# Kernel tuning notes

Hardware: AMD Instinct MI355X
Metric: run time of the kernel (lower is better)

## Reference

```python
import jax, jax.numpy as jnp
import numpy as np

EPS = 1e-5  # nn.LayerNorm default eps
N_LAYERS, N, D_IN, H, D_OUT, NH = 4, 2048, 512, 1024, 256, 16


def setup_inputs() -> dict:
    key = jax.random.key(0)
    ks = jax.random.split(key, 8)
    s = lambda k, shape: (jax.random.normal(k, shape, jnp.float32) * 0.02)
    return {
        "x": jax.random.normal(ks[0], (N, D_IN), jnp.float32),
        "W1": s(ks[1], (H, D_IN)), "b1": jnp.zeros((H,), jnp.float32),
        # per-layer MHA params, stacked on a leading layer axis
        "Wqkv": s(ks[2], (N_LAYERS, 3 * H, H)), "bqkv": jnp.zeros((N_LAYERS, 3 * H), jnp.float32),
        "Wo": s(ks[3], (N_LAYERS, H, H)), "bo": jnp.zeros((N_LAYERS, H), jnp.float32),
        "ln_g": jnp.ones((N_LAYERS, H), jnp.float32), "ln_b": jnp.zeros((N_LAYERS, H), jnp.float32),
        "W2": s(ks[4], (D_OUT, H)), "b2": jnp.zeros((D_OUT,), jnp.float32),
        "g_out": jnp.ones((D_OUT,), jnp.float32), "b_out": jnp.zeros((D_OUT,), jnp.float32),
        "num_heads": NH,
    }


def layer_norm(x, g, b):
    m = jnp.mean(x, axis=-1, keepdims=True)
    v = jnp.mean(jnp.square(x - m), axis=-1, keepdims=True)
    return (x - m) * jax.lax.rsqrt(v + EPS) * g + b


def mha(x, Wqkv, bqkv, Wo, bo, nh):
    # x: [N, H]; attention is over the N axis (torch MHA with batch_first=False, batch=1)
    n, h = x.shape
    hd = h // nh
    qkv = x @ Wqkv.T + bqkv                      # [N, 3H]
    q, k, v = jnp.split(qkv, 3, axis=-1)
    q = q.reshape(n, nh, hd).transpose(1, 0, 2)  # [nh, N, hd]
    k = k.reshape(n, nh, hd).transpose(1, 0, 2)
    v = v.reshape(n, nh, hd).transpose(1, 0, 2)
    scale = jnp.float32(1.0 / np.sqrt(hd))
    scores = jnp.einsum('hnd,hmd->hnm', q, k) * scale  # [nh, N, N]
    attn = jax.nn.softmax(scores, axis=-1)
    out = jnp.einsum('hnm,hmd->hnd', attn, v)          # [nh, N, hd]
    out = out.transpose(1, 0, 2).reshape(n, h)
    return out @ Wo.T + bo


def reference(x, W1, b1, Wqkv, bqkv, Wo, bo, ln_g, ln_b, W2, b2, g_out, b_out, num_heads):
    h = jax.nn.relu(x @ W1.T + b1)  # dropout is identity in eval mode
    for i in range(Wqkv.shape[0]):
        a = mha(h, Wqkv[i], bqkv[i], Wo[i], bo[i], num_heads)
        h = layer_norm(a + h, ln_g[i], ln_b[i])
    y = jax.nn.relu(h @ W2.T + b2)
    return layer_norm(y, g_out, b_out)
```

## Files before the change

### kernel.cpp

```cpp
#include <hip/hip_runtime.h>

typedef __attribute__((ext_vector_type(8))) short short8;
typedef __attribute__((ext_vector_type(4))) float f32x4;
typedef __attribute__((ext_vector_type(16))) float f32x16;
typedef __attribute__((ext_vector_type(4))) float float4v;
typedef __attribute__((ext_vector_type(4))) unsigned short ushort4v;
typedef __attribute__((ext_vector_type(4))) unsigned int uint4v;
typedef __attribute__((ext_vector_type(2))) unsigned int uint2v;

#define MFMA16(a, b, c) __builtin_amdgcn_mfma_f32_16x16x32_bf16((a), (b), (c), 0, 0, 0)
#define MFMA32(a, b, c) __builtin_amdgcn_mfma_f32_32x32x16_bf16((a), (b), (c), 0, 0, 0)
#define GLOAD_LDS16(g, s)                                                         \
  __builtin_amdgcn_global_load_lds((const __attribute__((address_space(1))) void*)(g), \
                                   (__attribute__((address_space(3))) void*)(s), 16, 0, 0)
#define EXP2(x) __builtin_amdgcn_exp2f(x)

__device__ __forceinline__ unsigned short f2bf(float f) {
  unsigned u = __builtin_bit_cast(unsigned, f);
  u += 0x7fffu + ((u >> 16) & 1u);
  return (unsigned short)(u >> 16);
}

__device__ __forceinline__ unsigned cvtpk(float lo, float hi) {
  unsigned r;
  asm("v_cvt_pk_bf16_f32 %0, %1, %2" : "=v"(r) : "v"(lo), "v"(hi));
  return r;
}

__device__ __forceinline__ void swap32(unsigned& a, unsigned& b) {
  asm volatile("v_permlane32_swap_b32 %0, %1" : "+v"(a), "+v"(b));
}

__device__ __forceinline__ float bflo(unsigned u) {
  return __builtin_bit_cast(float, u << 16);
}
__device__ __forceinline__ float bfhi(unsigned u) {
  return __builtin_bit_cast(float, u & 0xffff0000u);
}
__device__ __forceinline__ float bf2f(unsigned short u) {
  return __builtin_bit_cast(float, (unsigned)u << 16);
}

struct CvtArgs {
  const float* s[5];
  unsigned short* d[5];
  int off[6];
};

__global__ __launch_bounds__(256) void cvt_multi(CvtArgs a, int ntot4) {
  int i4 = blockIdx.x * 256 + threadIdx.x;
  const int stride = gridDim.x * 256;
  for (; i4 < ntot4; i4 += stride) {
    const int idx = i4 * 4;
    int s = 0;
#pragma unroll
    for (int k = 0; k < 4; ++k) s += (idx >= a.off[k + 1]) ? 1 : 0;
    const int local = idx - a.off[s];
    float4v v = *(const float4v*)(a.s[s] + local);
    ushort4v o;
    o.x = f2bf(v.x); o.y = f2bf(v.y); o.z = f2bf(v.z); o.w = f2bf(v.w);
    *(ushort4v*)(a.d[s] + local) = o;
  }
}

template <int BM, int BN, bool RELU, bool RES, bool OUTF, bool OUTB, bool OUTT>
__global__ __launch_bounds__(256) void gemm_bt(const unsigned short* __restrict__ A,
                                               const unsigned short* __restrict__ B,
                                               const float* __restrict__ bias,
                                               const unsigned short* __restrict__ resB,
                                               float* __restrict__ outF,
                                               unsigned short* __restrict__ outB,
                                               unsigned short* __restrict__ outT,
                                               int tcol0, int ldt,
                                               int M, int N, int K) {
  __shared__ __align__(16) unsigned short As[2][BM * 32];
  __shared__ __align__(16) unsigned short Bs[2][BN * 32];
  constexpr int MI = BM / 32, MJ = BN / 32, CA = BM / 64, CB = BN / 64;
  const int tid = threadIdx.x;
  const int w = tid >> 6, lane = tid & 63;
  const int l15 = lane & 15, l4 = lane >> 4;

  const int nwg = gridDim.x;
  const int wg = (blockIdx.x & 7) * (nwg >> 3) + (blockIdx.x >> 3);
  const int nbx = N / BN;
  const int rowBase = (wg / nbx) * BM;
  const int colBase = (wg % nbx) * BN;
  const int wm = w >> 1, wn = w & 1;

  f32x4 acc[MI][MJ] = {};

  auto stage = [&](int buf, int k0) {
#pragma unroll
    for (int i = 0; i < CA; ++i) {
      const int c = i * 256 + tid;
      GLOAD_LDS16(A + (size_t)(rowBase + (c >> 2)) * K + k0 + ((c & 3) << 3),
                  As[buf] + i * 2048 + w * 512);
    }
#pragma unroll
    for (int i = 0; i < CB; ++i) {
      const int c = i * 256 + tid;
      GLOAD_LDS16(B + (size_t)(colBase + (c >> 2)) * K + k0 + ((c & 3) << 3),
                  Bs[buf] + i * 2048 + w * 512);
    }
  };

  stage(0, 0);
  __syncthreads();

  int p = 0;
  for (int k0 = 0; k0 < K; k0 += 32) {
    if (k0 + 32 < K) stage(p ^ 1, k0 + 32);

    short8 af[MI], bf[MJ];
#pragma unroll
    for (int f = 0; f < MI; ++f)
      af[f] = *(const short8*)(As[p] + (wm * (BM / 2) + f * 16 + l15) * 32 + l4 * 8);
#pragma unroll
    for (int f = 0; f < MJ; ++f)
      bf[f] = *(const short8*)(Bs[p] + (wn * (BN / 2) + f * 16 + l15) * 32 + l4 * 8);
#pragma unroll
    for (int i = 0; i < MI; ++i)
#pragma unroll
      for (int j = 0; j < MJ; ++j)
        acc[i][j] = MFMA16(af[i], bf[j], acc[i][j]);

    __syncthreads();
    p ^= 1;
  }

#pragma unroll
  for (int i = 0; i < MI; ++i) {
    const int row0 = rowBase + wm * (BM / 2) + i * 16 + l4 * 4;
#pragma unroll
    for (int j = 0; j < MJ; ++j) {
      const int col = colBase + wn * (BN / 2) + j * 16 + l15;
      const float bv = bias[col];
      float vv[4];
#pragma unroll
      for (int e = 0; e < 4; ++e) {
        float v = acc[i][j][e] + bv;
        if constexpr (RELU) v = fmaxf(v, 0.f);
        if constexpr (RES) v += bf2f(resB[(size_t)(row0 + e) * N + col]);
        vv[e] = v;
        if constexpr (OUTF) outF[(size_t)(row0 + e) * N + col] = v;
        if constexpr (OUTB) outB[(size_t)(row0 + e) * N + col] = f2bf(v);
      }
      if constexpr (OUTT) {
        if (col >= tcol0) {
          ushort4v t;
          t.x = f2bf(vv[0]); t.y = f2bf(vv[1]); t.z = f2bf(vv[2]); t.w = f2bf(vv[3]);
          *(ushort4v*)(outT + (size_t)(col - tcol0) * ldt + row0) = t;
        }
      }
    }
  }
}

__global__ __launch_bounds__(256, 3) void flash_attn4(const unsigned short* __restrict__ qkv,
                                                      const unsigned short* __restrict__ vt,
                                                      unsigned short* __restrict__ Op0,
                                                      unsigned short* __restrict__ OpR,
                                                      float* __restrict__ Ml,
                                                      float* __restrict__ Ll,
                                                      int Nseq) {
  __shared__ __align__(16) unsigned short Ks[2][64 * 64];
  __shared__ __align__(16) unsigned short Vs[2][64 * 64];
  const int tid = threadIdx.x, w = tid >> 6, lane = tid & 63;
  const int l31 = lane & 31, l2h = lane >> 5, l7 = l31 & 7;
  const float CSC = 0.18033688011112042f;

  const int b = blockIdx.x;
  const int head = (b & 7) * 2 + ((b >> 3) & 1);
  const int s = (b >> 4) & 3;
  const int qb = b >> 6;
  const int q0w = qb * 128 + w * 32;

  const unsigned short* Qp = qkv + head * 64;
  const unsigned short* Kp = qkv + 1024 + head * 64;
  const unsigned short* Vtp = vt + (size_t)head * 64 * Nseq;

  short8 qf[4];
#pragma unroll
  for (int ka = 0; ka < 4; ++ka)
    qf[ka] = *(const short8*)(Qp + (size_t)(q0w + l31) * 3072 + ka * 16 + l2h * 8);

  f32x16 OT0 = {}, OT1 = {};
  float m = -1e30f, ls = 0.f;

  const int sr = tid >> 3, su = tid & 7;
  const int sOffA = sr * 64 + ((su ^ (sr & 7)) * 8);
  const int sOffB = sOffA + 32 * 64;

  const int kt0 = s * (Nseq >> 2);
  const int NIT = Nseq >> 8;

  short8 k0 = *(const short8*)(Kp + (size_t)(kt0 + sr) * 3072 + su * 8);
  short8 k1 = *(const short8*)(Kp + (size_t)(kt0 + sr + 32) * 3072 + su * 8);
  short8 v0 = *(const short8*)(Vtp + (size_t)sr * Nseq + kt0 + su * 8);
  short8 v1 = *(const short8*)(Vtp + (size_t)(sr + 32) * Nseq + kt0 + su * 8);
  *(short8*)(Ks[0] + sOffA) = k0;
  *(short8*)(Ks[0] + sOffB) = k1;
  *(short8*)(Vs[0] + sOffA) = v0;
  *(short8*)(Vs[0] + sOffB) = v1;
  __syncthreads();

  int p = 0;
  for (int it = 0; it < NIT; ++it) {
    const bool more = (it + 1) < NIT;
    if (more) {
      const int ktn = kt0 + (it + 1) * 64;
      k0 = *(const short8*)(Kp + (size_t)(ktn + sr) * 3072 + su * 8);
      k1 = *(const short8*)(Kp + (size_t)(ktn + sr + 32) * 3072 + su * 8);
      v0 = *(const short8*)(Vtp + (size_t)sr * Nseq + ktn + su * 8);
      v1 = *(const short8*)(Vtp + (size_t)(sr + 32) * Nseq + ktn + su * 8);
    }
    const unsigned short* KS = Ks[p];
    const unsigned short* VS = Vs[p];

    f32x16 S0 = {}, S1 = {};
    __builtin_amdgcn_s_setprio(1);
#pragma unroll
    for (int ka = 0; ka < 4; ++ka) {
      const int un = ((ka * 2 + l2h) ^ l7) * 8;
      const short8 a0 = *(const short8*)(KS + l31 * 64 + un);
      const short8 a1 = *(const short8*)(KS + (32 + l31) * 64 + un);
      S0 = MFMA32(a0, qf[ka], S0);
      S1 = MFMA32(a1, qf[ka], S1);
    }
    __builtin_amdgcn_s_setprio(0);

    float pm = S0[0];
#pragma unroll
    for (int r = 1; r < 16; ++r) pm = fmaxf(pm, S0[r]);
#pragma unroll
    for (int r = 0; r < 16; ++r) pm = fmaxf(pm, S1[r]);
    pm = fmaxf(pm, __shfl_xor(pm, 32));
    pm *= CSC;

    if (__any(pm > m + 8.f)) {
      const float mn = fmaxf(m, pm);
      const float fac = EXP2(m - mn);
      m = mn;
      ls *= fac;
#pragma unroll
      for (int r = 0; r < 16; ++r) { OT0[r] *= fac; OT1[r] *= fac; }
    }

    float rs = 0.f;
    unsigned W0[4][2], W1[4][2];
#pragma unroll
    for (int g = 0; g < 4; ++g) {
      const float a0 = EXP2(fmaf(S0[4 * g + 0], CSC, -m));
      const float a1 = EXP2(fmaf(S0[4 * g + 1], CSC, -m));
      const float a2 = EXP2(fmaf(S0[4 * g + 2], CSC, -m));
      const float a3 = EXP2(fmaf(S0[4 * g + 3], CSC, -m));
      const float b0 = EXP2(fmaf(S1[4 * g + 0], CSC, -m));
      const float b1 = EXP2(fmaf(S1[4 * g + 1], CSC, -m));
      const float b2 = EXP2(fmaf(S1[4 * g + 2], CSC, -m));
      const float b3 = EXP2(fmaf(S1[4 * g + 3], CSC, -m));
      rs += ((a0 + a1) + (a2 + a3)) + ((b0 + b1) + (b2 + b3));
      W0[g][0] = cvtpk(a0, a1); W0[g][1] = cvtpk(a2, a3);
      W1[g][0] = cvtpk(b0, b1); W1[g][1] = cvtpk(b2, b3);
    }
    rs += __shfl_xor(rs, 32);
    ls += rs;

    short8 pf[2][2];
#pragma unroll
    for (int ka = 0; ka < 2; ++ka) {
      {
        unsigned x0 = W0[2 * ka][0], y0 = W0[2 * ka + 1][0];
        unsigned x1 = W0[2 * ka][1], y1 = W0[2 * ka + 1][1];
        swap32(x0, y0);
        swap32(x1, y1);
        uint4v u = {x0, x1, y0, y1};
        pf[0][ka] = __builtin_bit_cast(short8, u);
      }
      {
        unsigned x0 = W1[2 * ka][0], y0 = W1[2 * ka + 1][0];
        unsigned x1 = W1[2 * ka][1], y1 = W1[2 * ka + 1][1];
        swap32(x0, y0);
        swap32(x1, y1);
        uint4v u = {x0, x1, y0, y1};
        pf[1][ka] = __builtin_bit_cast(short8, u);
      }
    }

    __builtin_amdgcn_s_setprio(1);
#pragma unroll
    for (int sub = 0; sub < 2; ++sub)
#pragma unroll
      for (int ka = 0; ka < 2; ++ka) {
        const int un = ((sub * 4 + ka * 2 + l2h) ^ l7) * 8;
        const short8 va0 = *(const short8*)(VS + l31 * 64 + un);
        const short8 va1 = *(const short8*)(VS + (32 + l31) * 64 + un);
        OT0 = MFMA32(va0, pf[sub][ka], OT0);
        OT1 = MFMA32(va1, pf[sub][ka], OT1);
      }
    __builtin_amdgcn_s_setprio(0);

    if (more) {
      unsigned short* Kn = Ks[p ^ 1];
      unsigned short* Vn = Vs[p ^ 1];
      *(short8*)(Kn + sOffA) = k0;
      *(short8*)(Kn + sOffB) = k1;
      *(short8*)(Vn + sOffA) = v0;
      *(short8*)(Vn + sOffB) = v1;
    }
    __syncthreads();
    p ^= 1;
  }

  unsigned short* Ob = (s == 0) ? Op0 : (OpR + (size_t)(s - 1) * Nseq * 1024);
  const int q = q0w + l31;
#pragma unroll
  for (int g = 0; g < 4; ++g) {
    const int d0 = 8 * g + 4 * l2h;
    uint2v t0 = {cvtpk(OT0[4 * g], OT0[4 * g + 1]), cvtpk(OT0[4 * g + 2], OT0[4 * g + 3])};
    uint2v t1 = {cvtpk(OT1[4 * g], OT1[4 * g + 1]), cvtpk(OT1[4 * g + 2], OT1[4 * g + 3])};
    *(uint2v*)(Ob + (size_t)q * 1024 + head * 64 + d0) = t0;
    *(uint2v*)(Ob + (size_t)q * 1024 + head * 64 + 32 + d0) = t1;
  }
  if (l2h == 0) {
    Ml[(size_t)(s * 16 + head) * Nseq + q] = m;
    Ll[(size_t)(s * 16 + head) * Nseq + q] = ls;
  }
}

__global__ __launch_bounds__(256) void attn_combine4(const unsigned short* __restrict__ Op0,
                                                     const unsigned short* __restrict__ OpR,
                                                     const float* __restrict__ Ml,
                                                     const float* __restrict__ Ll,
                                                     unsigned short* __restrict__ out, int Nseq) {
  const int t = blockIdx.x * 256 + threadIdx.x;
  const int q = t >> 8, c4 = (t & 255) * 4;
  const int head = c4 >> 6;
  float mm[4], lv[4];
  float M = -1e30f;
#pragma unroll
  for (int s = 0; s < 4; ++s) {
    mm[s] = Ml[(size_t)(s * 16 + head) * Nseq + q];
    lv[s] = Ll[(size_t)(s * 16 + head) * Nseq + q];
    M = fmaxf(M, mm[s]);
  }
  float denom = 0.f;
  float4v acc = {0.f, 0.f, 0.f, 0.f};
#pragma unroll
  for (int s = 0; s < 4; ++s) {
    const float ww = EXP2(mm[s] - M);
    denom += lv[s] * ww;
    const unsigned short* Ob = (s == 0) ? Op0 : (OpR + (size_t)(s - 1) * Nseq * 1024);
    uint2v o = *(const uint2v*)(Ob + (size_t)q * 1024 + c4);
    acc.x += bflo(o.x) * ww;
    acc.y += bfhi(o.x) * ww;
    acc.z += bflo(o.y) * ww;
    acc.w += bfhi(o.y) * ww;
  }
  const float inv = 1.f / denom;
  ushort4v r;
  r.x = f2bf(acc.x * inv);
  r.y = f2bf(acc.y * inv);
  r.z = f2bf(acc.z * inv);
  r.w = f2bf(acc.w * inv);
  *(ushort4v*)(out + (size_t)q * 1024 + c4) = r;
}

template <int D, bool WF, bool WB>
__global__ __launch_bounds__(256) void ln_rows(const float* __restrict__ src,
                                               const float* __restrict__ gw,
                                               const float* __restrict__ bw,
                                               float* __restrict__ outF,
                                               unsigned short* __restrict__ outB) {
  __shared__ float red[4];
  const int row = blockIdx.x;
  const int tid = threadIdx.x, w = tid >> 6;
  constexpr int PT = D / 256;
  const float* r = src + (size_t)row * D;
  float v[PT];
  float s = 0.f;
#pragma unroll
  for (int i = 0; i < PT; ++i) { v[i] = r[tid + i * 256]; s += v[i]; }
#pragma unroll
  for (int off = 32; off; off >>= 1) s += __shfl_down(s, off);
  if ((tid & 63) == 0) red[w] = s;
  __syncthreads();
  const float mean = (red[0] + red[1] + red[2] + red[3]) / D;
  __syncthreads();
  float q = 0.f;
#pragma unroll
  for (int i = 0; i < PT; ++i) { const float d = v[i] - mean; q += d * d; }
#pragma unroll
  for (int off = 32; off; off >>= 1) q += __shfl_down(q, off);
  if ((tid & 63) == 0) red[w] = q;
  __syncthreads();
  const float rstd = rsqrtf((red[0] + red[1] + red[2] + red[3]) / D + 1e-5f);
#pragma unroll
  for (int i = 0; i < PT; ++i) {
    const int c = tid + i * 256;
    const float o = (v[i] - mean) * rstd * gw[c] + bw[c];
    if constexpr (WF) outF[(size_t)row * D + c] = o;
    if constexpr (WB) outB[(size_t)row * D + c] = f2bf(o);
  }
}

extern "C" void kernel_launch(void* const* d_in, const int* in_sizes, int n_in,
                              void* d_out, int out_size, void* d_ws, size_t ws_size,
                              hipStream_t stream) {
  const int N = 2048, D_IN = 512, H = 1024, D_OUT = 256, NL = 4;
  const float* x    = (const float*)d_in[0];
  const float* W1   = (const float*)d_in[1];
  const float* b1   = (const float*)d_in[2];
  const float* Wqkv = (const float*)d_in[3];
  const float* bqkv = (const float*)d_in[4];
  const float* Wo   = (const float*)d_in[5];
  const float* bo   = (const float*)d_in[6];
  const float* lng  = (const float*)d_in[7];
  const float* lnb  = (const float*)d_in[8];
  const float* W2   = (const float*)d_in[9];
  const float* b2   = (const float*)d_in[10];
  const float* gout = (const float*)d_in[11];
  const float* bout = (const float*)d_in[12];
  float* out = (float*)d_out;

  char* ws = (char*)d_ws;
  auto alloc = [&](size_t bytes) -> char* {
    char* p = ws;
    ws += (bytes + 255) & ~(size_t)255;
    return p;
  };
  unsigned short* xb    = (unsigned short*)alloc((size_t)N * D_IN * 2);
  unsigned short* W1b   = (unsigned short*)alloc((size_t)H * D_IN * 2);
  unsigned short* Wqkvb = (unsigned short*)alloc((size_t)NL * 3 * H * H * 2);
  unsigned short* Wob   = (unsigned short*)alloc((size_t)NL * H * H * 2);
  unsigned short* W2b   = (unsigned short*)alloc((size_t)D_OUT * H * 2);
  unsigned short* hb    = (unsigned short*)alloc((size_t)N * H * 2);
  unsigned short* qkvb  = (unsigned short*)alloc((size_t)N * 3 * H * 2);
  unsigned short* aob   = (unsigned short*)alloc((size_t)N * H * 2);
  unsigned short* vtg   = (unsigned short*)alloc((size_t)H * N * 2);
  unsigned short* opb0  = (unsigned short*)alloc((size_t)N * H * 2);
  unsigned short* opbR  = (unsigned short*)alloc((size_t)3 * N * H * 2);
  float* af  = (float*)alloc((size_t)N * H * 4);
  float* ml  = (float*)alloc((size_t)4 * 16 * N * 4);
  float* ll  = (float*)alloc((size_t)4 * 16 * N * 4);
  float* yf  = (float*)alloc((size_t)N * D_OUT * 4);

  CvtArgs ca;
  ca.s[0] = x;    ca.d[0] = xb;
  ca.s[1] = W1;   ca.d[1] = W1b;
  ca.s[2] = Wqkv; ca.d[2] = Wqkvb;
  ca.s[3] = Wo;   ca.d[3] = Wob;
  ca.s[4] = W2;   ca.d[4] = W2b;
  const int n0 = N * D_IN, n1 = H * D_IN, n2 = NL * 3 * H * H, n3 = NL * H * H, n4 = D_OUT * H;
  ca.off[0] = 0;
  ca.off[1] = n0;
  ca.off[2] = n0 + n1;
  ca.off[3] = n0 + n1 + n2;
  ca.off[4] = n0 + n1 + n2 + n3;
  ca.off[5] = n0 + n1 + n2 + n3 + n4;
  const int ntot4 = ca.off[5] / 4;
  cvt_multi<<<2048, 256, 0, stream>>>(ca, ntot4);

  gemm_bt<64, 64, true, false, false, true, false><<<(N / 64) * (H / 64), 256, 0, stream>>>(
      xb, W1b, b1, nullptr, nullptr, hb, nullptr, 0, 0, N, H, D_IN);

  for (int l = 0; l < NL; ++l) {
    gemm_bt<128, 128, false, false, false, true, true><<<(N / 128) * (3 * H / 128), 256, 0, stream>>>(
        hb, Wqkvb + (size_t)l * 3 * H * H, bqkv + (size_t)l * 3 * H, nullptr, nullptr, qkvb,
        vtg, 2 * H, N, N, 3 * H, H);
    flash_attn4<<<1024, 256, 0, stream>>>(qkvb, vtg, opb0, opbR, ml, ll, N);
    attn_combine4<<<(N * H / 4) / 256, 256, 0, stream>>>(opb0, opbR, ml, ll, aob, N);
    gemm_bt<64, 64, false, true, true, false, false><<<(N / 64) * (H / 64), 256, 0, stream>>>(
        aob, Wob + (size_t)l * H * H, bo + (size_t)l * H, hb, af, nullptr, nullptr, 0, 0,
        N, H, H);
    ln_rows<1024, false, true><<<N, 256, 0, stream>>>(af, lng + (size_t)l * H,
                                                      lnb + (size_t)l * H, nullptr, hb);
  }

  gemm_bt<64, 64, true, false, true, false, false><<<(N / 64) * (D_OUT / 64), 256, 0, stream>>>(
      hb, W2b, b2, nullptr, yf, nullptr, nullptr, 0, 0, N, D_OUT, H);
  ln_rows<256, true, false><<<N, 256, 0, stream>>>(yf, gout, bout, out, nullptr);
}
```

Before: 383.0 us.

## Fuse split-KV attention combine into flash kernel via in-block LDS reduction

The four KV-split partial attentions now run as four wave-groups inside one 1024-thread block rather than as separate blocks. Their softmax statistics are shared through LDS, and the rescaled partial outputs are summed with LDS atomic adds before a single bf16 write. This removes the separate combine kernel, one launch per layer, and the global round trip of the partial outputs and max/sum buffers. In exchange, the grid drops from 1024 to 256 blocks, LDS use per block grows, block-wide barriers are added, and float atomics go to shared memory.

After: 515.6 us. 34.6% more time.

```diff
diff --git a/kernel.cpp b/kernel.cpp
--- a/kernel.cpp
+++ b/kernel.cpp
@@ -31,12 +31,6 @@
   asm volatile("v_permlane32_swap_b32 %0, %1" : "+v"(a), "+v"(b));
 }
 
-__device__ __forceinline__ float bflo(unsigned u) {
-  return __builtin_bit_cast(float, u << 16);
-}
-__device__ __forceinline__ float bfhi(unsigned u) {
-  return __builtin_bit_cast(float, u & 0xffff0000u);
-}
 __device__ __forceinline__ float bf2f(unsigned short u) {
   return __builtin_bit_cast(float, (unsigned)u << 16);
 }
@@ -156,24 +150,25 @@
   }
 }
 
-__global__ __launch_bounds__(256, 3) void flash_attn4(const unsigned short* __restrict__ qkv,
-                                                      const unsigned short* __restrict__ vt,
-                                                      unsigned short* __restrict__ Op0,
-                                                      unsigned short* __restrict__ OpR,
-                                                      float* __restrict__ Ml,
-                                                      float* __restrict__ Ll,
-                                                      int Nseq) {
-  __shared__ __align__(16) unsigned short Ks[2][64 * 64];
-  __shared__ __align__(16) unsigned short Vs[2][64 * 64];
-  const int tid = threadIdx.x, w = tid >> 6, lane = tid & 63;
+__global__ __launch_bounds__(1024, 4) void flash_attn6(const unsigned short* __restrict__ qkv,
+                                                       const unsigned short* __restrict__ vt,
+                                                       unsigned short* __restrict__ aout,
+                                                       int Nseq) {
+  __shared__ __align__(16) unsigned short KsAll[4 * 2 * 64 * 64];
+  __shared__ __align__(16) unsigned short VsAll[4 * 2 * 64 * 64];
+  __shared__ float mArr[4][4][32];
+  __shared__ float lArr[4][4][32];
+
+  const int tid = threadIdx.x;
+  const int ws = tid >> 6, lane = tid & 63;
+  const int qsub = ws & 3, s = ws >> 2;
   const int l31 = lane & 31, l2h = lane >> 5, l7 = l31 & 7;
   const float CSC = 0.18033688011112042f;
 
   const int b = blockIdx.x;
   const int head = (b & 7) * 2 + ((b >> 3) & 1);
-  const int s = (b >> 4) & 3;
-  const int qb = b >> 6;
-  const int q0w = qb * 128 + w * 32;
+  const int qt = b >> 4;
+  const int q0w = qt * 128 + qsub * 32;
 
   const unsigned short* Qp = qkv + head * 64;
   const unsigned short* Kp = qkv + 1024 + head * 64;
@@ -187,9 +182,12 @@
   f32x16 OT0 = {}, OT1 = {};
   float m = -1e30f, ls = 0.f;
 
-  const int sr = tid >> 3, su = tid & 7;
+  const int t2 = qsub * 64 + lane;
+  const int sr = t2 >> 3, su = t2 & 7;
   const int sOffA = sr * 64 + ((su ^ (sr & 7)) * 8);
   const int sOffB = sOffA + 32 * 64;
+  unsigned short* Ksb = KsAll + s * 2 * 4096;
+  unsigned short* Vsb = VsAll + s * 2 * 4096;
 
   const int kt0 = s * (Nseq >> 2);
   const int NIT = Nseq >> 8;
@@ -198,10 +196,10 @@
   short8 k1 = *(const short8*)(Kp + (size_t)(kt0 + sr + 32) * 3072 + su * 8);
   short8 v0 = *(const short8*)(Vtp + (size_t)sr * Nseq + kt0 + su * 8);
   short8 v1 = *(const short8*)(Vtp + (size_t)(sr + 32) * Nseq + kt0 + su * 8);
-  *(short8*)(Ks[0] + sOffA) = k0;
-  *(short8*)(Ks[0] + sOffB) = k1;
-  *(short8*)(Vs[0] + sOffA) = v0;
-  *(short8*)(Vs[0] + sOffB) = v1;
+  *(short8*)(Ksb + sOffA) = k0;
+  *(short8*)(Ksb + sOffB) = k1;
+  *(short8*)(Vsb + sOffA) = v0;
+  *(short8*)(Vsb + sOffB) = v1;
   __syncthreads();
 
   int p = 0;
@@ -214,8 +212,8 @@
       v0 = *(const short8*)(Vtp + (size_t)sr * Nseq + ktn + su * 8);
       v1 = *(const short8*)(Vtp + (size_t)(sr + 32) * Nseq + ktn + su * 8);
     }
-    const unsigned short* KS = Ks[p];
-    const unsigned short* VS = Vs[p];
+    const unsigned short* KS = Ksb + p * 4096;
+    const unsigned short* VS = Vsb + p * 4096;
 
     f32x16 S0 = {}, S1 = {};
     __builtin_amdgcn_s_setprio(1);
@@ -300,8 +298,8 @@
     __builtin_amdgcn_s_setprio(0);
 
     if (more) {
-      unsigned short* Kn = Ks[p ^ 1];
-      unsigned short* Vn = Vs[p ^ 1];
+      unsigned short* Kn = Ksb + (p ^ 1) * 4096;
+      unsigned short* Vn = Vsb + (p ^ 1) * 4096;
       *(short8*)(Kn + sOffA) = k0;
       *(short8*)(Kn + sOffB) = k1;
       *(short8*)(Vn + sOffA) = v0;
@@ -311,58 +309,46 @@
     p ^= 1;
   }
 
-  unsigned short* Ob = (s == 0) ? Op0 : (OpR + (size_t)(s - 1) * Nseq * 1024);
-  const int q = q0w + l31;
-#pragma unroll
-  for (int g = 0; g < 4; ++g) {
-    const int d0 = 8 * g + 4 * l2h;
-    uint2v t0 = {cvtpk(OT0[4 * g], OT0[4 * g + 1]), cvtpk(OT0[4 * g + 2], OT0[4 * g + 3])};
-    uint2v t1 = {cvtpk(OT1[4 * g], OT1[4 * g + 1]), cvtpk(OT1[4 * g + 2], OT1[4 * g + 3])};
-    *(uint2v*)(Ob + (size_t)q * 1024 + head * 64 + d0) = t0;
-    *(uint2v*)(Ob + (size_t)q * 1024 + head * 64 + 32 + d0) = t1;
-  }
-  if (l2h == 0) {
-    Ml[(size_t)(s * 16 + head) * Nseq + q] = m;
-    Ll[(size_t)(s * 16 + head) * Nseq + q] = ls;
-  }
-}
-
-__global__ __launch_bounds__(256) void attn_combine4(const unsigned short* __restrict__ Op0,
-                                                     const unsigned short* __restrict__ OpR,
-                                                     const float* __restrict__ Ml,
-                                                     const float* __restrict__ Ll,
-                                                     unsigned short* __restrict__ out, int Nseq) {
-  const int t = blockIdx.x * 256 + threadIdx.x;
-  const int q = t >> 8, c4 = (t & 255) * 4;
-  const int head = c4 >> 6;
-  float mm[4], lv[4];
-  float M = -1e30f;
-#pragma unroll
-  for (int s = 0; s < 4; ++s) {
-    mm[s] = Ml[(size_t)(s * 16 + head) * Nseq + q];
-    lv[s] = Ll[(size_t)(s * 16 + head) * Nseq + q];
-    M = fmaxf(M, mm[s]);
-  }
+  if (l2h == 0) { mArr[s][qsub][l31] = m; lArr[s][qsub][l31] = ls; }
+  __syncthreads();
+  const float M = fmaxf(fmaxf(mArr[0][qsub][l31], mArr[1][qsub][l31]),
+                        fmaxf(mArr[2][qsub][l31], mArr[3][qsub][l31]));
   float denom = 0.f;
-  float4v acc = {0.f, 0.f, 0.f, 0.f};
-#pragma unroll
-  for (int s = 0; s < 4; ++s) {
-    const float ww = EXP2(mm[s] - M);
-    denom += lv[s] * ww;
-    const unsigned short* Ob = (s == 0) ? Op0 : (OpR + (size_t)(s - 1) * Nseq * 1024);
-    uint2v o = *(const uint2v*)(Ob + (size_t)q * 1024 + c4);
-    acc.x += bflo(o.x) * ww;
-    acc.y += bfhi(o.x) * ww;
-    acc.z += bflo(o.y) * ww;
-    acc.w += bfhi(o.y) * ww;
-  }
-  const float inv = 1.f / denom;
-  ushort4v r;
-  r.x = f2bf(acc.x * inv);
-  r.y = f2bf(acc.y * inv);
-  r.z = f2bf(acc.z * inv);
-  r.w = f2bf(acc.w * inv);
-  *(ushort4v*)(out + (size_t)q * 1024 + c4) = r;
+#pragma unroll
+  for (int s2 = 0; s2 < 4; ++s2)
+    denom += lArr[s2][qsub][l31] * EXP2(mArr[s2][qsub][l31] - M);
+  const float scale = EXP2(m - M) / denom;
+
+  float* acc = (float*)KsAll;
+  for (int i = tid; i < 8192; i += 1024) acc[i] = 0.f;
+  __syncthreads();
+
+  const int rowbase = (qsub * 32 + l31) * 64;
+  const int xorv = (l31 & 7) << 2;
+#pragma unroll
+  for (int g = 0; g < 4; ++g)
+#pragma unroll
+    for (int e = 0; e < 4; ++e) {
+      const int d = 8 * g + 4 * l2h + e;
+      atomicAdd(acc + rowbase + (d ^ xorv), OT0[4 * g + e] * scale);
+      atomicAdd(acc + rowbase + ((d + 32) ^ xorv), OT1[4 * g + e] * scale);
+    }
+  __syncthreads();
+
+  const int i0 = tid * 8;
+  const int qr = i0 >> 6;
+  const int dstart = i0 & 63;
+  const int xq = (qr & 7) << 2;
+  float vr[8];
+#pragma unroll
+  for (int j = 0; j < 8; ++j)
+    vr[j] = acc[qr * 64 + ((dstart + j) ^ xq)];
+  uint4v o;
+  o.x = cvtpk(vr[0], vr[1]);
+  o.y = cvtpk(vr[2], vr[3]);
+  o.z = cvtpk(vr[4], vr[5]);
+  o.w = cvtpk(vr[6], vr[7]);
+  *(uint4v*)(aout + (size_t)(qt * 128 + qr) * 1024 + head * 64 + dstart) = o;
 }
 
 template <int D, bool WF, bool WB>
@@ -437,11 +423,7 @@
   unsigned short* qkvb  = (unsigned short*)alloc((size_t)N * 3 * H * 2);
   unsigned short* aob   = (unsigned short*)alloc((size_t)N * H * 2);
   unsigned short* vtg   = (unsigned short*)alloc((size_t)H * N * 2);
-  unsigned short* opb0  = (unsigned short*)alloc((size_t)N * H * 2);
-  unsigned short* opbR  = (unsigned short*)alloc((size_t)3 * N * H * 2);
   float* af  = (float*)alloc((size_t)N * H * 4);
-  float* ml  = (float*)alloc((size_t)4 * 16 * N * 4);
-  float* ll  = (float*)alloc((size_t)4 * 16 * N * 4);
   float* yf  = (float*)alloc((size_t)N * D_OUT * 4);
 
   CvtArgs ca;
@@ -467,8 +449,7 @@
     gemm_bt<128, 128, false, false, false, true, true><<<(N / 128) * (3 * H / 128), 256, 0, stream>>>(
         hb, Wqkvb + (size_t)l * 3 * H * H, bqkv + (size_t)l * 3 * H, nullptr, nullptr, qkvb,
         vtg, 2 * H, N, N, 3 * H, H);
-    flash_attn4<<<1024, 256, 0, stream>>>(qkvb, vtg, opb0, opbR, ml, ll, N);
-    attn_combine4<<<(N * H / 4) / 256, 256, 0, stream>>>(opb0, opbR, ml, ll, aob, N);
+    flash_attn6<<<256, 1024, 0, stream>>>(qkvb, vtg, aob, N);
     gemm_bt<64, 64, false, true, true, false, false><<<(N / 64) * (H / 64), 256, 0, stream>>>(
         aob, Wob + (size_t)l * H * H, bo + (size_t)l * H, hb, af, nullptr, nullptr, 0, 0,
         N, H, H);
```
